# Kernel tuning notes

Measured on AMD Instinct MI355X. Metric: run time of the kernel, lower is better.

The kernel has to match this reference:

```python
import jax, jax.numpy as jnp
import numpy as np

N_HEAD = 12
MIN_SIZE = 4
MAX_SIZE = 8
TOP_M = 16
ALPHA = 1.0
EPS = 1e-6
NEG_INF = -1e30


def setup_inputs() -> dict:
    key = jax.random.key(0)
    ks = jax.random.split(key, 4)
    B, T, C = 2, 512, 768
    x = jax.random.normal(ks[0], (B, T, C), jnp.float32)
    w_qkv = jax.random.normal(ks[1], (C, 3 * C), jnp.float32) * (1.0 / np.sqrt(C))
    b_qkv = jnp.zeros((3 * C,), jnp.float32)
    w_proj = jax.random.normal(ks[2], (C, C), jnp.float32) * (1.0 / np.sqrt(C))
    b_proj = jnp.zeros((C,), jnp.float32)
    gate_param = jnp.zeros((), jnp.float32)  # dpp_gate_init = 0.0 -> gate = 0.5
    return {"x": x, "w_qkv": w_qkv, "b_qkv": b_qkv, "w_proj": w_proj,
            "b_proj": b_proj, "gate_param": gate_param}


def _dpp_token(i, q_i, k, v):
    """Greedy DPP subset selection + attention for one query token.
    q_i: [hd], k/v: [T, hd]. Faithful to the torch greedy loop, vectorized
    over candidates with incremental Gram construction (scores only gate the
    discrete selection, so they are computed under stop_gradient, matching
    torch where they only feed Python comparisons)."""
    T, hd = k.shape
    kc = jax.lax.stop_gradient(k)
    qc = jax.lax.stop_gradient(q_i)
    # causal similarity, topk candidates
    sim = jnp.where(jnp.arange(T) <= i, kc @ qc, NEG_INF)
    _, topidx = jax.lax.top_k(sim, TOP_M)  # [M]
    # candidates = top-min(TOP_M, i+1) causal neighbors, excluding i itself
    cand_active = (jnp.arange(TOP_M) < jnp.minimum(TOP_M, i + 1)) & (topidx != i)
    cand_keys = kc[topidx]                              # [M, hd]
    cnorm = jnp.sum(cand_keys * cand_keys, axis=-1)     # [M]

    sel_idx = jnp.zeros((MAX_SIZE,), jnp.int32).at[0].set(i)
    sel_count = jnp.int32(1)
    # initial score: log(det([k_i.k_i]) + eps) / 1**alpha
    cur = jnp.log(jnp.dot(kc[i], kc[i]) + EPS)
    stopped = jnp.bool_(False)
    eye = jnp.eye(MAX_SIZE, dtype=jnp.float32)
    slots = jnp.arange(MAX_SIZE)

    for _ in range(MAX_SIZE - 1):
        rowmask = slots < sel_count                       # [S] current subset rows
        pos = (slots == sel_count).astype(jnp.float32)    # slot for new candidate
        Ksel = kc[sel_idx] * rowmask[:, None].astype(jnp.float32)  # [S, hd]
        G0 = Ksel @ Ksel.T                                # [S, S]
        cross = cand_keys @ Ksel.T                        # [M, S]
        # Gc[c,a,b] = G0[a,b] + pos[a]*cross[c,b] + pos[b]*cross[c,a] + pos[a]pos[b]*cnorm[c]
        Gc = (G0[None]
              + pos[None, :, None] * cross[:, None, :]
              + pos[None, None, :] * cross[:, :, None]
              + (pos[:, None] * pos[None, :])[None] * cnorm[:, None, None])
        newmask = rowmask | (slots == sel_count)
        # identity-pad unused rows/cols so det equals det of the active submatrix
        Gc = Gc + (eye * (1.0 - newmask.astype(jnp.float32)))[None]
        dets = jnp.linalg.det(Gc)                         # [M] (float32, as torch)
        size = (sel_count + 1).astype(jnp.float32)
        score = jnp.log(dets + EPS) / size ** ALPHA       # minimize_det=False
        masked = jnp.where(cand_active, score, NEG_INF)
        best = jnp.argmax(masked)
        best_score = masked[best]
        any_cand = jnp.any(cand_active)
        take = any_cand & (~stopped) & ((best_score > cur) | (sel_count < MIN_SIZE))
        sel_idx = jnp.where(take, sel_idx.at[sel_count].set(topidx[best].astype(jnp.int32)), sel_idx)
        cand_active = jnp.where(take, cand_active.at[best].set(False), cand_active)
        cur = jnp.where(take, best_score, cur)
        sel_count = sel_count + take.astype(jnp.int32)
        stopped = stopped | (~take)

    # attention over the selected subset (gradients flow through k, v, q here)
    rowmask = slots < sel_count
    Ks = k[sel_idx]
    Vs = v[sel_idx]
    logits = jnp.where(rowmask, (Ks @ q_i) / np.float32(np.sqrt(hd)), NEG_INF)
    w = jax.nn.softmax(logits)
    return w @ Vs


def _forward(x, w_qkv, b_qkv, w_proj, b_proj, gate_param):
    B, T, C = x.shape
    hd = C // N_HEAD
    qkv = x @ w_qkv + b_qkv
    q, k, v = jnp.split(qkv, 3, axis=-1)

    def heads(t):  # [B,T,C] -> [B*NH, T, hd]
        return t.reshape(B, T, N_HEAD, hd).transpose(0, 2, 1, 3).reshape(B * N_HEAD, T, hd)

    q, k, v = heads(q), heads(k), heads(v)

    # standard causal softmax attention (flash path, dropout=0 at eval)
    scale = np.float32(1.0 / np.sqrt(hd))
    att = jnp.einsum('nqd,nkd->nqk', q, k) * scale
    causal = jnp.tril(jnp.ones((T, T), bool))
    att = jnp.where(causal[None], att, NEG_INF)
    y_std = jnp.einsum('nqk,nkd->nqd', jax.nn.softmax(att, axis=-1), v)

    # DPP greedy-selection attention, vmapped over tokens and (batch*head)
    dpp_head = jax.vmap(_dpp_token, in_axes=(0, 0, None, None))
    y_dpp = jax.vmap(lambda qh, kh, vh: dpp_head(jnp.arange(T), qh, kh, vh))(q, k, v)

    gate = jax.nn.sigmoid(gate_param)
    y = gate * y_dpp + (1.0 - gate) * y_std
    y = y.reshape(B, N_HEAD, T, hd).transpose(0, 2, 1, 3).reshape(B, T, C)
    return y @ w_proj + b_proj


def reference(x, w_qkv, b_qkv, w_proj, b_proj, gate_param):
    return _forward(x, w_qkv, b_qkv, w_proj, b_proj, gate_param)
```

## Files before the change

kernel.cpp:

```cpp
#include <hip/hip_runtime.h>
#include <math.h>

constexpr int SEQ   = 512;
constexpr int HDIM  = 64;
constexpr int NHEAD = 12;
constexpr int NBATCH = 2;
constexpr int CDIM  = 768;
constexpr int TOPM  = 16;
constexpr int SMAX  = 8;
constexpr float NEGINF = -1e30f;

typedef short bf16x8 __attribute__((ext_vector_type(8)));
typedef float f32x4  __attribute__((ext_vector_type(4)));

__device__ inline void gload_lds16(const void* src, void* lds_base)
{
    __builtin_amdgcn_global_load_lds(
        (const __attribute__((address_space(1))) void*)src,
        (__attribute__((address_space(3))) void*)lds_base, 16, 0, 0);
}

__device__ inline unsigned short f2bf(float f)
{
    unsigned u = __float_as_uint(f);
    return (unsigned short)((u + 0x7FFFu + ((u >> 16) & 1u)) >> 16);
}
__device__ inline float bf2f(unsigned short h)
{
    return __uint_as_float((unsigned)h << 16);
}
__device__ inline void split3(float f, unsigned short& h,
                              unsigned short& m, unsigned short& l)
{
    h = f2bf(f);
    float r1 = f - bf2f(h);
    m = f2bf(r1);
    l = f2bf(r1 - bf2f(m));
}

__global__ __launch_bounds__(256) void split_x_kernel(
    const float* __restrict__ x, unsigned short* __restrict__ xh,
    unsigned short* __restrict__ xm, unsigned short* __restrict__ xl)
{
    const int idx = (blockIdx.x * 256 + threadIdx.x) * 4;
    float4 v = *(const float4*)(x + idx);
    float vv[4] = {v.x, v.y, v.z, v.w};
    unsigned short h[4], m[4], l[4];
    #pragma unroll
    for (int e = 0; e < 4; ++e) split3(vv[e], h[e], m[e], l[e]);
    *(ushort4*)(xh + idx) = make_ushort4(h[0], h[1], h[2], h[3]);
    *(ushort4*)(xm + idx) = make_ushort4(m[0], m[1], m[2], m[3]);
    *(ushort4*)(xl + idx) = make_ushort4(l[0], l[1], l[2], l[3]);
}

__global__ __launch_bounds__(256) void tsplit_w_kernel(
    const float* __restrict__ w, unsigned short* __restrict__ wh,
    unsigned short* __restrict__ wm, unsigned short* __restrict__ wl)
{
    __shared__ float T[64][65];
    const int c0 = blockIdx.x * 64;
    const int k0 = blockIdx.y * 64;
    const int tid = threadIdx.x;
    #pragma unroll
    for (int i = 0; i < 16; ++i) {
        int idx = tid + i * 256;
        int kk = idx >> 6, cc = idx & 63;
        T[kk][cc] = w[(size_t)(k0 + kk) * (3 * CDIM) + c0 + cc];
    }
    __syncthreads();
    #pragma unroll
    for (int i = 0; i < 16; ++i) {
        int idx = tid + i * 256;
        int col = idx >> 6, kk = idx & 63;
        unsigned short h, m, l;
        split3(T[kk][col], h, m, l);
        size_t o = (size_t)(c0 + col) * CDIM + k0 + kk;
        wh[o] = h; wm[o] = m; wl[o] = l;
    }
}

__global__ __launch_bounds__(256) void qkv_mfma_kernel(
    const unsigned short* __restrict__ xh, const unsigned short* __restrict__ xm,
    const unsigned short* __restrict__ xl, const unsigned short* __restrict__ wh,
    const unsigned short* __restrict__ wm, const unsigned short* __restrict__ wl,
    const float* __restrict__ bias,
    float* __restrict__ q, float* __restrict__ k, float* __restrict__ v)
{
    __shared__ unsigned short As[3][64 * 32];
    __shared__ unsigned short Bs[3][64 * 32];
    const int bn = blockIdx.x * 64;
    const int bm = blockIdx.y * 64;
    const int tid = threadIdx.x;
    const int wid = tid >> 6;
    const int lane = tid & 63;
    const int lrow = lane & 15;
    const int lk8 = (lane >> 4) << 3;

    f32x4 acc[4];
    #pragma unroll
    for (int b = 0; b < 4; ++b) acc[b] = (f32x4){0.f, 0.f, 0.f, 0.f};

    const unsigned short* xs[3] = {xh, xm, xl};
    const unsigned short* wsrc[3] = {wh, wm, wl};

    const int slot = wid * 64 + lane;
    const int srow = slot >> 2;
    const int sk8 = (slot & 3) << 3;

    for (int k0 = 0; k0 < CDIM; k0 += 32) {
        #pragma unroll
        for (int c = 0; c < 3; ++c)
            gload_lds16(xs[c] + (size_t)(bm + srow) * CDIM + k0 + sk8,
                        &As[c][wid * 512]);
        #pragma unroll
        for (int c = 0; c < 3; ++c)
            gload_lds16(wsrc[c] + (size_t)(bn + srow) * CDIM + k0 + sk8,
                        &Bs[c][wid * 512]);
        __syncthreads();

        bf16x8 bf[3][4];
        #pragma unroll
        for (int c = 0; c < 3; ++c)
            #pragma unroll
            for (int ni = 0; ni < 4; ++ni)
                bf[c][ni] = *(const bf16x8*)&Bs[c][(ni * 16 + lrow) * 32 + lk8];

        bf16x8 ah = *(const bf16x8*)&As[0][(wid * 16 + lrow) * 32 + lk8];
        bf16x8 am = *(const bf16x8*)&As[1][(wid * 16 + lrow) * 32 + lk8];
        bf16x8 al = *(const bf16x8*)&As[2][(wid * 16 + lrow) * 32 + lk8];
        #pragma unroll
        for (int ni = 0; ni < 4; ++ni) {
            f32x4 a = acc[ni];
            a = __builtin_amdgcn_mfma_f32_16x16x32_bf16(al, bf[0][ni], a, 0, 0, 0);
            a = __builtin_amdgcn_mfma_f32_16x16x32_bf16(ah, bf[2][ni], a, 0, 0, 0);
            a = __builtin_amdgcn_mfma_f32_16x16x32_bf16(am, bf[1][ni], a, 0, 0, 0);
            a = __builtin_amdgcn_mfma_f32_16x16x32_bf16(am, bf[0][ni], a, 0, 0, 0);
            a = __builtin_amdgcn_mfma_f32_16x16x32_bf16(ah, bf[1][ni], a, 0, 0, 0);
            a = __builtin_amdgcn_mfma_f32_16x16x32_bf16(ah, bf[0][ni], a, 0, 0, 0);
            acc[ni] = a;
        }
        __syncthreads();
    }

    const int rbase = (lane >> 4) << 2;
    #pragma unroll
    for (int ni = 0; ni < 4; ++ni) {
        int cc = bn + ni * 16 + lrow;
        float bval = bias[cc];
        int part = cc / CDIM;
        int c2 = cc - part * CDIM;
        int hh = c2 >> 6, d = c2 & 63;
        float* dst = (part == 0) ? q : ((part == 1) ? k : v);
        #pragma unroll
        for (int r = 0; r < 4; ++r) {
            int m = bm + wid * 16 + rbase + r;
            int b_ = m >> 9, t = m & 511;
            dst[((((size_t)b_ * NHEAD + hh) * SEQ) + t) * HDIM + d] =
                acc[ni][r] + bval;
        }
    }
}

__global__ __launch_bounds__(256) void qkkt_mfma_kernel(
    const float* __restrict__ q, const float* __restrict__ k,
    float* __restrict__ S, float* __restrict__ KKT)
{
    __shared__ float Qs[64 * 32];
    __shared__ float Kas[64 * 32];
    __shared__ float Kbs[64 * 32];
    const int e = blockIdx.x;
    const int n = blockIdx.y;
    int it = 0, start = 0;
    while (start + it + 1 <= e) { start += it + 1; ++it; }
    const int jt = e - start;
    const int tid = threadIdx.x;
    const int wid = tid >> 6;
    const int lane = tid & 63;
    const int lrow = lane & 15;
    const int lk8 = (lane >> 4) << 3;
    const float* qh = q + (size_t)n * SEQ * HDIM;
    const float* kh = k + (size_t)n * SEQ * HDIM;

    f32x4 accS[4], accG[4];
    #pragma unroll
    for (int b = 0; b < 4; ++b) {
        accS[b] = (f32x4){0.f, 0.f, 0.f, 0.f};
        accG[b] = (f32x4){0.f, 0.f, 0.f, 0.f};
    }

    #pragma unroll
    for (int ks = 0; ks < 2; ++ks) {
        const int k0 = ks * 32;
        #pragma unroll
        for (int l = 0; l < 2; ++l) {
            int g = l * 256 + wid * 64 + lane;
            int r = g >> 3, f4 = (g & 7) << 2;
            float* dstQ = Qs + (l * 256 + wid * 64) * 4;
            float* dstA = Kas + (l * 256 + wid * 64) * 4;
            float* dstB = Kbs + (l * 256 + wid * 64) * 4;
            gload_lds16(qh + (size_t)(it * 64 + r) * HDIM + k0 + f4, dstQ);
            gload_lds16(kh + (size_t)(it * 64 + r) * HDIM + k0 + f4, dstA);
            gload_lds16(kh + (size_t)(jt * 64 + r) * HDIM + k0 + f4, dstB);
        }
        __syncthreads();

        bf16x8 qfh, qfm, qfl, afh, afm, afl;
        {
            const float* qr = Qs + (wid * 16 + lrow) * 32 + lk8;
            const float* ar = Kas + (wid * 16 + lrow) * 32 + lk8;
            #pragma unroll
            for (int e2 = 0; e2 < 8; ++e2) {
                unsigned short h, m, l;
                split3(qr[e2], h, m, l);
                qfh[e2] = (short)h; qfm[e2] = (short)m; qfl[e2] = (short)l;
                split3(ar[e2], h, m, l);
                afh[e2] = (short)h; afm[e2] = (short)m; afl[e2] = (short)l;
            }
        }
        bf16x8 bfh[4], bfm[4], bfl[4];
        #pragma unroll
        for (int ni = 0; ni < 4; ++ni) {
            const float* br = Kbs + (ni * 16 + lrow) * 32 + lk8;
            #pragma unroll
            for (int e2 = 0; e2 < 8; ++e2) {
                unsigned short h, m, l;
                split3(br[e2], h, m, l);
                bfh[ni][e2] = (short)h; bfm[ni][e2] = (short)m; bfl[ni][e2] = (short)l;
            }
        }
        #pragma unroll
        for (int ni = 0; ni < 4; ++ni) {
            f32x4 a = accS[ni];
            a = __builtin_amdgcn_mfma_f32_16x16x32_bf16(qfl, bfh[ni], a, 0, 0, 0);
            a = __builtin_amdgcn_mfma_f32_16x16x32_bf16(qfh, bfl[ni], a, 0, 0, 0);
            a = __builtin_amdgcn_mfma_f32_16x16x32_bf16(qfm, bfm[ni], a, 0, 0, 0);
            a = __builtin_amdgcn_mfma_f32_16x16x32_bf16(qfm, bfh[ni], a, 0, 0, 0);
            a = __builtin_amdgcn_mfma_f32_16x16x32_bf16(qfh, bfm[ni], a, 0, 0, 0);
            a = __builtin_amdgcn_mfma_f32_16x16x32_bf16(qfh, bfh[ni], a, 0, 0, 0);
            accS[ni] = a;
            f32x4 g = accG[ni];
            g = __builtin_amdgcn_mfma_f32_16x16x32_bf16(afl, bfh[ni], g, 0, 0, 0);
            g = __builtin_amdgcn_mfma_f32_16x16x32_bf16(afh, bfl[ni], g, 0, 0, 0);
            g = __builtin_amdgcn_mfma_f32_16x16x32_bf16(afm, bfm[ni], g, 0, 0, 0);
            g = __builtin_amdgcn_mfma_f32_16x16x32_bf16(afm, bfh[ni], g, 0, 0, 0);
            g = __builtin_amdgcn_mfma_f32_16x16x32_bf16(afh, bfm[ni], g, 0, 0, 0);
            g = __builtin_amdgcn_mfma_f32_16x16x32_bf16(afh, bfh[ni], g, 0, 0, 0);
            accG[ni] = g;
        }
        __syncthreads();
    }

    const int rbase = (lane >> 4) << 2;
    float* gdst = KKT + ((size_t)n * 36 + e) * 4096;
    #pragma unroll
    for (int ni = 0; ni < 4; ++ni) {
        int coll = ni * 16 + lrow;
        int col = jt * 64 + coll;
        #pragma unroll
        for (int r = 0; r < 4; ++r) {
            int rowl = wid * 16 + rbase + r;
            int row = it * 64 + rowl;
            S[((size_t)n * SEQ + row) * SEQ + col] = accS[ni][r];
            gdst[rowl * 64 + coll] = accG[ni][r];
        }
    }
}

__device__ inline double hybrid_log(double a)
{
    unsigned long long b = __double_as_longlong(a);
    int e2 = (int)((b >> 52) & 0x7FF) - 1022;
    double m = __longlong_as_double((b & 0x000FFFFFFFFFFFFFULL) |
                                    0x3FE0000000000000ULL);
    return ((double)__log2f((float)m) + (double)e2) * 0.6931471805599453;
}

__device__ inline double rsqrt64(double x)
{
    double r = (double)rsqrtf((float)x);
    r = r * (1.5 - 0.5 * x * r * r);
    return r;
}

#define CSW(a, b)                                                        \
    {                                                                    \
        bool sw = (v##a < v##b) || ((v##a == v##b) && (j##a > j##b));    \
        float tf = sw ? v##b : v##a;                                     \
        float uf = sw ? v##a : v##b;                                     \
        int ti = sw ? j##b : j##a;                                       \
        int ui = sw ? j##a : j##b;                                       \
        v##a = tf; v##b = uf; j##a = ti; j##b = ui;                      \
    }

__global__ __launch_bounds__(128) void dpp_kernel(
    const float* __restrict__ v, float* __restrict__ S,
    const float* __restrict__ KKT, const float* __restrict__ gate_p,
    float* __restrict__ y, float* __restrict__ denomArr)
{
    const int tid  = threadIdx.x;
    const int wid  = tid >> 6;
    const int lane = tid & 63;
    const int i = blockIdx.x * 2 + wid;
    const int n = blockIdx.y;
    const float* vh = v + (size_t)n * SEQ * HDIM;
    const float* KKTh = KKT + (size_t)n * 36 * 4096;
    float* Srow = S + ((size_t)n * SEQ + i) * SEQ;

    __shared__ float prow[2][SEQ];
    __shared__ float gramf[2][17][17];
    __shared__ int   eidx[2][17];
    __shared__ int   selS[2][SMAX];

    float sim8[8];
    #pragma unroll
    for (int m = 0; m < 8; ++m) {
        int j = lane + (m << 6);
        sim8[m] = (j <= i) ? Srow[j] : NEGINF;
    }
    if (lane < SMAX) selS[wid][lane] = i;

    {
        float v0 = sim8[0], v1 = sim8[1], v2 = sim8[2], v3 = sim8[3],
              v4 = sim8[4], v5 = sim8[5], v6 = sim8[6], v7 = sim8[7];
        int j0 = lane, j1 = lane + 64, j2 = lane + 128, j3 = lane + 192,
            j4 = lane + 256, j5 = lane + 320, j6 = lane + 384, j7 = lane + 448;
        CSW(0, 1) CSW(2, 3) CSW(4, 5) CSW(6, 7)
        CSW(0, 2) CSW(1, 3) CSW(4, 6) CSW(5, 7)
        CSW(1, 2) CSW(5, 6)
        CSW(0, 4) CSW(1, 5) CSW(2, 6) CSW(3, 7)
        CSW(2, 4) CSW(3, 5)
        CSW(1, 2) CSW(3, 4) CSW(5, 6)

        if (lane == 0) eidx[wid][0] = i;
        #pragma unroll
        for (int s = 0; s < TOPM; ++s) {
            float rv = v0;
            #pragma unroll
            for (int off = 32; off; off >>= 1)
                rv = fmaxf(rv, __shfl_xor(rv, off));
            unsigned long long tied = __ballot(v0 == rv);
            int ri;
            if (__popcll(tied) == 1) {
                ri = __shfl(j0, (int)__builtin_ctzll(tied));
            } else {
                int cnd = (v0 == rv) ? j0 : 0x7FFFFFFF;
                #pragma unroll
                for (int off = 32; off; off >>= 1)
                    cnd = min(cnd, __shfl_xor(cnd, off));
                ri = cnd;
            }
            if (lane == 0) eidx[wid][1 + s] = ri;
            if (v0 == rv && j0 == ri) {
                v0 = v1; j0 = j1; v1 = v2; j1 = j2; v2 = v3; j2 = j3;
                v3 = v4; j3 = j4; v4 = v5; j4 = j5; v5 = v6; j5 = j6;
                v6 = v7; j6 = j7; v7 = -3e38f; j7 = 1023;
            }
        }
    }

    const float scale = 0.125f;
    float lm = -3e38f;
    #pragma unroll
    for (int m = 0; m < 8; ++m) lm = fmaxf(lm, sim8[m]);
    #pragma unroll
    for (int off = 32; off; off >>= 1) lm = fmaxf(lm, __shfl_xor(lm, off));
    const float mx = lm * scale;
    float sum = 0.f;
    #pragma unroll
    for (int m = 0; m < 8; ++m) {
        float p = expf(sim8[m] * scale - mx);
        int j = lane + (m << 6);
        prow[wid][j] = p;
        Srow[j] = p;
        sum += p;
    }
    #pragma unroll
    for (int off = 32; off; off >>= 1) sum += __shfl_xor(sum, off);
    const float denom = sum;
    asm volatile("s_waitcnt lgkmcnt(0)" ::: "memory");

    for (int e = lane; e < 153; e += 64) {
        int a = (int)((sqrtf(8.f * (float)e + 1.f) - 1.f) * 0.5f);
        int st = (a * (a + 1)) >> 1;
        if (st > e) { --a; st = (a * (a + 1)) >> 1; }
        else if (st + a + 1 <= e) { ++a; st = (a * (a + 1)) >> 1; }
        int b = e - st;
        int ra = eidx[wid][a], rb = eidx[wid][b];
        int row = ra > rb ? ra : rb;
        int col = ra > rb ? rb : ra;
        int itt = row >> 6, jtt = col >> 6;
        int p = ((itt * (itt + 1)) >> 1) + jtt;
        float s = KKTh[((size_t)p * 64 + (row & 63)) * 64 + (col & 63)];
        gramf[wid][a][b] = s;
        gramf[wid][b][a] = s;
    }
    asm volatile("s_waitcnt lgkmcnt(0)" ::: "memory");

    int sc = 1;
    {
        const int c = lane;
        const bool isCand = (c < TOPM);
        const int nvalid = (i + 1 < TOPM) ? (i + 1) : TOPM;
        bool active = isCand && (c < nvalid) && (eidx[wid][1 + c] != i);
        double zc[7];
        #pragma unroll
        for (int t = 0; t < 7; ++t) zc[t] = 0.0;
        double det = (double)gramf[wid][0][0];
        double cur = 0.0;
        double invL00 = rsqrt64(det > 0.0 ? det : 1e-30);
        double dcv = 0.0;
        if (isCand) {
            zc[0] = (double)gramf[wid][1 + c][0] * invL00;
            dcv = (double)gramf[wid][1 + c][1 + c] - zc[0] * zc[0];
        }

        for (int it2 = 0; it2 < SMAX - 1; ++it2) {
            double argc = det * dcv + 1e-6;
            double key = active ? (argc > 0.0 ? argc : 1e300) : -1.0;
            int rc = c;
            #pragma unroll
            for (int off = 1; off <= 8; off <<= 1) {
                double ov = __shfl_xor(key, off);
                int    oc = __shfl_xor(rc, off);
                if (ov > key || (ov == key && oc < rc)) { key = ov; rc = oc; }
            }
            rc = __shfl(rc, 0);
            bool any = (__any(active ? 1 : 0) != 0);
            double dbest = __shfl(dcv, rc);
            bool take;
            if (it2 < 2) {
                take = any;
            } else {
                double argb = det * dbest + 1e-6;
                bool pos = argb > 0.0;
                double score = hybrid_log(pos ? argb : 1.0) / (double)(sc + 1);
                take = any && (it2 < 3 || (pos && score > cur));
                if (take) cur = pos ? score : __builtin_nan("");
            }
            if (!take) break;

            double invLss = rsqrt64(dbest > 1e-30 ? dbest : 1e-30);
            double zb[7];
            #pragma unroll
            for (int t = 0; t < 7; ++t) zb[t] = __shfl(zc[t], rc);
            if (isCand) {
                double crossn = (double)gramf[wid][1 + c][1 + rc];
                double s2 = 0.0;
                #pragma unroll
                for (int t = 0; t < 7; ++t) s2 += zc[t] * zb[t];
                double znew = (crossn - s2) * invLss;
                #pragma unroll
                for (int t = 0; t < 7; ++t) if (t == sc) zc[t] = znew;
                dcv -= znew * znew;
            }
            det = det * dbest;
            if (c == rc) active = false;
            if (lane == 0) selS[wid][sc] = eidx[wid][1 + rc];
            ++sc;
        }
    }

    int selI[SMAX];
    #pragma unroll
    for (int s = 0; s < SMAX; ++s) selI[s] = selS[wid][s];
    float wsum = 0.f;
    #pragma unroll
    for (int s = 0; s < SMAX; ++s) if (s < sc) wsum += prow[wid][selI[s]];
    float yd = 0.f;
    #pragma unroll
    for (int s = 0; s < SMAX; ++s)
        if (s < sc) yd = fmaf(prow[wid][selI[s]], vh[selI[s] * HDIM + lane], yd);
    const float gp = gate_p[0];
    const float gate = 1.f / (1.f + expf(-gp));
    y[((size_t)n * SEQ + i) * HDIM + lane] = gate * yd / wsum;
    if (lane == 0) denomArr[n * SEQ + i] = denom;
}

__global__ __launch_bounds__(256) void pv_gemm_kernel(
    const float* __restrict__ P, const float* __restrict__ v,
    const float* __restrict__ denomArr, const float* __restrict__ gate_p,
    float* __restrict__ y)
{
    __shared__ float Ps[32][36];
    __shared__ float Vs[32][68];
    const int tt = blockIdx.x;
    const int n  = blockIdx.y;
    const int t0 = tt * 32;
    const int tid = threadIdx.x;
    const float* Ph = P + (size_t)n * SEQ * SEQ;
    const float* vh = v + (size_t)n * SEQ * HDIM;
    const int tm = (tid >> 4) << 1;
    const int tn = (tid & 15) << 2;
    float acc[2][4] = {};
    const int jmax = t0 + 32;
    for (int j0 = 0; j0 < jmax; j0 += 32) {
        {
            int tok = tid >> 3, j4 = (tid & 7) << 2;
            *(float4*)&Ps[tok][j4] =
                *(const float4*)(Ph + (t0 + tok) * SEQ + j0 + j4);
        }
        #pragma unroll
        for (int l = 0; l < 2; ++l) {
            int idx = tid + l * 256;
            int j = idx >> 4, d4 = (idx & 15) << 2;
            *(float4*)&Vs[j][d4] = *(const float4*)(vh + (j0 + j) * HDIM + d4);
        }
        __syncthreads();
        #pragma unroll
        for (int j4 = 0; j4 < 8; ++j4) {
            float4 p0r = *(const float4*)&Ps[tm + 0][j4 << 2];
            float4 p1r = *(const float4*)&Ps[tm + 1][j4 << 2];
            float pr[2][4] = {{p0r.x, p0r.y, p0r.z, p0r.w},
                              {p1r.x, p1r.y, p1r.z, p1r.w}};
            #pragma unroll
            for (int l = 0; l < 4; ++l) {
                float4 v4 = *(const float4*)&Vs[(j4 << 2) + l][tn];
                float vv[4] = {v4.x, v4.y, v4.z, v4.w};
                #pragma unroll
                for (int u = 0; u < 2; ++u)
                    #pragma unroll
                    for (int w2 = 0; w2 < 4; ++w2)
                        acc[u][w2] = fmaf(pr[u][l], vv[w2], acc[u][w2]);
            }
        }
        __syncthreads();
    }
    const float gp = gate_p[0];
    const float gate = 1.f / (1.f + expf(-gp));
    #pragma unroll
    for (int u = 0; u < 2; ++u) {
        int i = t0 + tm + u;
        float den = denomArr[n * SEQ + i];
        #pragma unroll
        for (int w2 = 0; w2 < 4; ++w2) {
            int d = tn + w2;
            size_t off = ((size_t)n * SEQ + i) * HDIM + d;
            y[off] += (1.f - gate) * acc[u][w2] / den;
        }
    }
}

__global__ __launch_bounds__(256) void proj_gemm_kernel(
    const float* __restrict__ y, const float* __restrict__ w,
    float* __restrict__ partial)
{
    __shared__ float As[128][36];
    __shared__ float Bs[32][68];
    const int bm = blockIdx.y * 128;
    const int bn = blockIdx.x * 64;
    const int kbase = blockIdx.z * 96;
    const int tid = threadIdx.x;
    const int tm = (tid >> 4) << 3;
    const int tn = (tid & 15) << 2;
    const int blk = tid >> 3;
    const int bln = (tid & 7) << 3;

    float acc[8][4] = {};
    for (int t = 0; t < 3; ++t) {
        const int k0 = kbase + t * 32;
        float4 av[4];
        #pragma unroll
        for (int l = 0; l < 4; ++l) {
            int idx = tid + l * 256;
            int row = bm + (idx >> 3);
            int col = k0 + ((idx & 7) << 2);
            int b_ = row >> 9, tk = row & 511;
            int h = col >> 6, d = col & 63;
            av[l] = *(const float4*)(y + ((((size_t)b_ * NHEAD + h) * SEQ) + tk) * HDIM + d);
        }
        float4 b0 = *(const float4*)(w + (k0 + blk) * CDIM + bn + bln);
        float4 b1 = *(const float4*)(w + (k0 + blk) * CDIM + bn + bln + 4);
        #pragma unroll
        for (int l = 0; l < 4; ++l) {
            int idx = tid + l * 256;
            int row = idx >> 3, kq = (idx & 7) << 2;
            *(float4*)&As[row][kq] = av[l];
        }
        *(float4*)&Bs[blk][bln] = b0;
        *(float4*)&Bs[blk][bln + 4] = b1;
        __syncthreads();
        #pragma unroll
        for (int k4 = 0; k4 < 8; ++k4) {
            float ar[8][4];
            #pragma unroll
            for (int u = 0; u < 8; ++u) {
                float4 a4 = *(const float4*)&As[tm + u][k4 << 2];
                ar[u][0] = a4.x; ar[u][1] = a4.y;
                ar[u][2] = a4.z; ar[u][3] = a4.w;
            }
            #pragma unroll
            for (int j = 0; j < 4; ++j) {
                float4 b4 = *(const float4*)&Bs[(k4 << 2) + j][tn];
                float bb[4] = {b4.x, b4.y, b4.z, b4.w};
                #pragma unroll
                for (int u = 0; u < 8; ++u)
                    #pragma unroll
                    for (int w2 = 0; w2 < 4; ++w2)
                        acc[u][w2] = fmaf(ar[u][j], bb[w2], acc[u][w2]);
            }
        }
        __syncthreads();
    }
    float* dst = partial + (size_t)blockIdx.z * (1024 * 768);
    #pragma unroll
    for (int u = 0; u < 8; ++u) {
        float4 o = {acc[u][0], acc[u][1], acc[u][2], acc[u][3]};
        *(float4*)(dst + (size_t)(bm + tm + u) * 768 + bn + tn) = o;
    }
}

__global__ __launch_bounds__(256) void proj_reduce_kernel(
    const float* __restrict__ partial, const float* __restrict__ bias,
    float* __restrict__ out)
{
    const int idx = blockIdx.x * 256 + threadIdx.x;
    const int m = idx / 192;
    const int cc = (idx - m * 192) << 2;
    const size_t MN = (size_t)1024 * 768;
    float4 s = *(const float4*)(partial + (size_t)m * 768 + cc);
    #pragma unroll
    for (int z = 1; z < 8; ++z) {
        float4 p = *(const float4*)(partial + (size_t)z * MN + (size_t)m * 768 + cc);
        s.x += p.x; s.y += p.y; s.z += p.z; s.w += p.w;
    }
    float4 b4 = *(const float4*)(bias + cc);
    float4 o = {s.x + b4.x, s.y + b4.y, s.z + b4.z, s.w + b4.w};
    *(float4*)(out + (size_t)m * 768 + cc) = o;
}

extern "C" void kernel_launch(void* const* d_in, const int* in_sizes, int n_in,
                              void* d_out, int out_size, void* d_ws, size_t ws_size,
                              hipStream_t stream)
{
    const float* x      = (const float*)d_in[0];
    const float* w_qkv  = (const float*)d_in[1];
    const float* b_qkv  = (const float*)d_in[2];
    const float* w_proj = (const float*)d_in[3];
    const float* b_proj = (const float*)d_in[4];
    const float* gate_p = (const float*)d_in[5];
    float* out = (float*)d_out;

    float* ws = (float*)d_ws;
    const size_t HS = (size_t)NBATCH * NHEAD * SEQ * HDIM;
    const size_t SS = (size_t)NBATCH * NHEAD * SEQ * SEQ;
    float* q   = ws;
    float* k   = q + HS;
    float* v   = k + HS;
    float* y   = v + HS;
    float* S   = y + HS;
    float* den = S + SS;
    float* KKT = den + 16384;

    unsigned short* us = (unsigned short*)S;
    unsigned short* xh = us;
    unsigned short* xm = us + 786432;
    unsigned short* xl = us + 1572864;
    unsigned short* wh = us + 2359296;
    unsigned short* wm = us + 2359296 + 1769472;
    unsigned short* wl = us + 2359296 + 3538944;

    split_x_kernel<<<768, 256, 0, stream>>>(x, xh, xm, xl);
    tsplit_w_kernel<<<dim3(36, 12), 256, 0, stream>>>(w_qkv, wh, wm, wl);
    qkv_mfma_kernel<<<dim3(36, 16), 256, 0, stream>>>(
        xh, xm, xl, wh, wm, wl, b_qkv, q, k, v);
    qkkt_mfma_kernel<<<dim3(36, NBATCH * NHEAD), 256, 0, stream>>>(q, k, S, KKT);
    dpp_kernel<<<dim3(SEQ / 2, NBATCH * NHEAD), 128, 0, stream>>>(
        v, S, KKT, gate_p, y, den);
    pv_gemm_kernel<<<dim3(SEQ / 32, NBATCH * NHEAD), 256, 0, stream>>>(
        S, v, den, gate_p, y);
    proj_gemm_kernel<<<dim3(CDIM / 64, (NBATCH * SEQ) / 128, 8), 256, 0, stream>>>(
        y, w_proj, S);
    proj_reduce_kernel<<<768, 256, 0, stream>>>(S, b_proj, out);
}
```

Baseline: 164.0 us.

## Replace split-K FP32 output projection with bf16x3 MFMA kernel

The output projection was a split-K FP32 FMA GEMM that wrote eight partial buffers and then ran a separate reduction kernel. It is replaced by a single MFMA kernel that splits y into three bf16 parts on the fly, uses pre-split bf16 triplets of w_proj, and adds the bias directly. A transposing split kernel for w_proj is launched earlier, reusing q's workspace after the QK kernel has consumed it. This removes the partial-sum traffic and the extra launch. It depends on the bf16x3 split matching FP32 accuracy and on q's buffer no longer being read once the QK kernel finishes.

```diff
diff --git a/kernel.cpp b/kernel.cpp
--- a/kernel.cpp
+++ b/kernel.cpp
@@ -53,8 +53,8 @@
     *(ushort4*)(xl + idx) = make_ushort4(l[0], l[1], l[2], l[3]);
 }
 
-__global__ __launch_bounds__(256) void tsplit_w_kernel(
-    const float* __restrict__ w, unsigned short* __restrict__ wh,
+__global__ __launch_bounds__(256) void tsplit_kernel(
+    const float* __restrict__ w, int ncols, unsigned short* __restrict__ wh,
     unsigned short* __restrict__ wm, unsigned short* __restrict__ wl)
 {
     __shared__ float T[64][65];
@@ -65,7 +65,7 @@
     for (int i = 0; i < 16; ++i) {
         int idx = tid + i * 256;
         int kk = idx >> 6, cc = idx & 63;
-        T[kk][cc] = w[(size_t)(k0 + kk) * (3 * CDIM) + c0 + cc];
+        T[kk][cc] = w[(size_t)(k0 + kk) * ncols + c0 + cc];
     }
     __syncthreads();
     #pragma unroll
@@ -540,92 +540,90 @@
     }
 }
 
-__global__ __launch_bounds__(256) void proj_gemm_kernel(
-    const float* __restrict__ y, const float* __restrict__ w,
-    float* __restrict__ partial)
-{
-    __shared__ float As[128][36];
-    __shared__ float Bs[32][68];
-    const int bm = blockIdx.y * 128;
+__global__ __launch_bounds__(256) void proj_mfma_kernel(
+    const float* __restrict__ y, const unsigned short* __restrict__ wh,
+    const unsigned short* __restrict__ wm, const unsigned short* __restrict__ wl,
+    const float* __restrict__ bias, float* __restrict__ out)
+{
+    __shared__ float Ys[64 * 32];
+    __shared__ unsigned short Bs[3][64 * 32];
     const int bn = blockIdx.x * 64;
-    const int kbase = blockIdx.z * 96;
+    const int bm = blockIdx.y * 64;
     const int tid = threadIdx.x;
-    const int tm = (tid >> 4) << 3;
-    const int tn = (tid & 15) << 2;
-    const int blk = tid >> 3;
-    const int bln = (tid & 7) << 3;
-
-    float acc[8][4] = {};
-    for (int t = 0; t < 3; ++t) {
-        const int k0 = kbase + t * 32;
-        float4 av[4];
-        #pragma unroll
-        for (int l = 0; l < 4; ++l) {
-            int idx = tid + l * 256;
-            int row = bm + (idx >> 3);
-            int col = k0 + ((idx & 7) << 2);
-            int b_ = row >> 9, tk = row & 511;
-            int h = col >> 6, d = col & 63;
-            av[l] = *(const float4*)(y + ((((size_t)b_ * NHEAD + h) * SEQ) + tk) * HDIM + d);
-        }
-        float4 b0 = *(const float4*)(w + (k0 + blk) * CDIM + bn + bln);
-        float4 b1 = *(const float4*)(w + (k0 + blk) * CDIM + bn + bln + 4);
-        #pragma unroll
-        for (int l = 0; l < 4; ++l) {
-            int idx = tid + l * 256;
-            int row = idx >> 3, kq = (idx & 7) << 2;
-            *(float4*)&As[row][kq] = av[l];
-        }
-        *(float4*)&Bs[blk][bln] = b0;
-        *(float4*)&Bs[blk][bln + 4] = b1;
-        __syncthreads();
-        #pragma unroll
-        for (int k4 = 0; k4 < 8; ++k4) {
-            float ar[8][4];
-            #pragma unroll
-            for (int u = 0; u < 8; ++u) {
-                float4 a4 = *(const float4*)&As[tm + u][k4 << 2];
-                ar[u][0] = a4.x; ar[u][1] = a4.y;
-                ar[u][2] = a4.z; ar[u][3] = a4.w;
-            }
-            #pragma unroll
-            for (int j = 0; j < 4; ++j) {
-                float4 b4 = *(const float4*)&Bs[(k4 << 2) + j][tn];
-                float bb[4] = {b4.x, b4.y, b4.z, b4.w};
-                #pragma unroll
-                for (int u = 0; u < 8; ++u)
-                    #pragma unroll
-                    for (int w2 = 0; w2 < 4; ++w2)
-                        acc[u][w2] = fmaf(ar[u][j], bb[w2], acc[u][w2]);
-            }
-        }
-        __syncthreads();
-    }
-    float* dst = partial + (size_t)blockIdx.z * (1024 * 768);
-    #pragma unroll
-    for (int u = 0; u < 8; ++u) {
-        float4 o = {acc[u][0], acc[u][1], acc[u][2], acc[u][3]};
-        *(float4*)(dst + (size_t)(bm + tm + u) * 768 + bn + tn) = o;
-    }
-}
-
-__global__ __launch_bounds__(256) void proj_reduce_kernel(
-    const float* __restrict__ partial, const float* __restrict__ bias,
-    float* __restrict__ out)
-{
-    const int idx = blockIdx.x * 256 + threadIdx.x;
-    const int m = idx / 192;
-    const int cc = (idx - m * 192) << 2;
-    const size_t MN = (size_t)1024 * 768;
-    float4 s = *(const float4*)(partial + (size_t)m * 768 + cc);
-    #pragma unroll
-    for (int z = 1; z < 8; ++z) {
-        float4 p = *(const float4*)(partial + (size_t)z * MN + (size_t)m * 768 + cc);
-        s.x += p.x; s.y += p.y; s.z += p.z; s.w += p.w;
-    }
-    float4 b4 = *(const float4*)(bias + cc);
-    float4 o = {s.x + b4.x, s.y + b4.y, s.z + b4.z, s.w + b4.w};
-    *(float4*)(out + (size_t)m * 768 + cc) = o;
+    const int wid = tid >> 6;
+    const int lane = tid & 63;
+    const int lrow = lane & 15;
+    const int lk8 = (lane >> 4) << 3;
+
+    f32x4 acc[4];
+    #pragma unroll
+    for (int b = 0; b < 4; ++b) acc[b] = (f32x4){0.f, 0.f, 0.f, 0.f};
+
+    const unsigned short* wsrc[3] = {wh, wm, wl};
+    const int bslot = wid * 64 + lane;
+    const int bcol = bslot >> 2;
+    const int bk8 = (bslot & 3) << 3;
+
+    for (int k0 = 0; k0 < CDIM; k0 += 32) {
+        #pragma unroll
+        for (int l = 0; l < 2; ++l) {
+            int g = l * 256 + wid * 64 + lane;
+            int r = g >> 3, f4 = (g & 7) << 2;
+            int m = bm + r;
+            int col = k0 + f4;
+            int b_ = m >> 9, t = m & 511;
+            int hh = col >> 6, d = col & 63;
+            gload_lds16(y + ((((size_t)b_ * NHEAD + hh) * SEQ) + t) * HDIM + d,
+                        Ys + (l * 256 + wid * 64) * 4);
+        }
+        #pragma unroll
+        for (int c = 0; c < 3; ++c)
+            gload_lds16(wsrc[c] + (size_t)(bn + bcol) * CDIM + k0 + bk8,
+                        &Bs[c][wid * 512]);
+        __syncthreads();
+
+        bf16x8 afh, afm, afl;
+        {
+            const float* ar = Ys + (wid * 16 + lrow) * 32 + lk8;
+            #pragma unroll
+            for (int e2 = 0; e2 < 8; ++e2) {
+                unsigned short h, m, l;
+                split3(ar[e2], h, m, l);
+                afh[e2] = (short)h; afm[e2] = (short)m; afl[e2] = (short)l;
+            }
+        }
+        bf16x8 bf[3][4];
+        #pragma unroll
+        for (int c = 0; c < 3; ++c)
+            #pragma unroll
+            for (int ni = 0; ni < 4; ++ni)
+                bf[c][ni] = *(const bf16x8*)&Bs[c][(ni * 16 + lrow) * 32 + lk8];
+
+        #pragma unroll
+        for (int ni = 0; ni < 4; ++ni) {
+            f32x4 a = acc[ni];
+            a = __builtin_amdgcn_mfma_f32_16x16x32_bf16(afl, bf[0][ni], a, 0, 0, 0);
+            a = __builtin_amdgcn_mfma_f32_16x16x32_bf16(afh, bf[2][ni], a, 0, 0, 0);
+            a = __builtin_amdgcn_mfma_f32_16x16x32_bf16(afm, bf[1][ni], a, 0, 0, 0);
+            a = __builtin_amdgcn_mfma_f32_16x16x32_bf16(afm, bf[0][ni], a, 0, 0, 0);
+            a = __builtin_amdgcn_mfma_f32_16x16x32_bf16(afh, bf[1][ni], a, 0, 0, 0);
+            a = __builtin_amdgcn_mfma_f32_16x16x32_bf16(afh, bf[0][ni], a, 0, 0, 0);
+            acc[ni] = a;
+        }
+        __syncthreads();
+    }
+
+    const int rbase = (lane >> 4) << 2;
+    #pragma unroll
+    for (int ni = 0; ni < 4; ++ni) {
+        int cc = bn + ni * 16 + lrow;
+        float bval = bias[cc];
+        #pragma unroll
+        for (int r = 0; r < 4; ++r) {
+            int m = bm + wid * 16 + rbase + r;
+            out[(size_t)m * CDIM + cc] = acc[ni][r] + bval;
+        }
+    }
 }
 
 extern "C" void kernel_launch(void* const* d_in, const int* in_sizes, int n_in,
@@ -659,16 +657,21 @@
     unsigned short* wm = us + 2359296 + 1769472;
     unsigned short* wl = us + 2359296 + 3538944;
 
+    unsigned short* qk = (unsigned short*)ws;
+    unsigned short* wph = qk;
+    unsigned short* wpm = qk + 589824;
+    unsigned short* wpl = qk + 2 * 589824;
+
     split_x_kernel<<<768, 256, 0, stream>>>(x, xh, xm, xl);
-    tsplit_w_kernel<<<dim3(36, 12), 256, 0, stream>>>(w_qkv, wh, wm, wl);
+    tsplit_kernel<<<dim3(36, 12), 256, 0, stream>>>(w_qkv, 3 * CDIM, wh, wm, wl);
     qkv_mfma_kernel<<<dim3(36, 16), 256, 0, stream>>>(
         xh, xm, xl, wh, wm, wl, b_qkv, q, k, v);
     qkkt_mfma_kernel<<<dim3(36, NBATCH * NHEAD), 256, 0, stream>>>(q, k, S, KKT);
+    tsplit_kernel<<<dim3(12, 12), 256, 0, stream>>>(w_proj, CDIM, wph, wpm, wpl);
     dpp_kernel<<<dim3(SEQ / 2, NBATCH * NHEAD), 128, 0, stream>>>(
         v, S, KKT, gate_p, y, den);
     pv_gemm_kernel<<<dim3(SEQ / 32, NBATCH * NHEAD), 256, 0, stream>>>(
         S, v, den, gate_p, y);
-    proj_gemm_kernel<<<dim3(CDIM / 64, (NBATCH * SEQ) / 128, 8), 256, 0, stream>>>(
-        y, w_proj, S);
-    proj_reduce_kernel<<<768, 256, 0, stream>>>(S, b_proj, out);
-}
+    proj_mfma_kernel<<<dim3(12, 16), 256, 0, stream>>>(
+        y, wph, wpm, wpl, b_proj, out);
+}
```

Result: no change. 166.2 us (+1.3%).
